# Optimization experiments

Hardware: AMD Instinct MI355X
Metric: run time of the kernel (lower is better)

Reference implementation:

```python
import jax, jax.numpy as jnp
import numpy as np

DIM_IN = 256
DIM = 256      # dim_out
N = 4096       # nodes at current depth
K = 16         # max children (padded)
R = 8192       # rows in previous-level h/c tensors (row 0 is the zero init row)


def _reverse_sequence(x, length):
    """TF reverse_sequence along axis 1: reverse first length[i] steps, keep tail."""
    T = x.shape[1]
    t = jnp.arange(T)
    idx = jnp.where(t[None, :] < length[:, None], length[:, None] - 1 - t[None, :], t[None, :])
    return jnp.take_along_axis(x, idx[:, :, None], axis=1)


def _lstm(x, kernel, rec, bias, h0, c0):
    """Standard (CuDNN/Keras gate order i,f,g,o) LSTM. x: [B,T,D] -> y: [B,T,H]."""
    xz = jnp.einsum('btd,dg->btg', x, kernel) + bias  # precompute input projection

    def step(carry, xz_t):
        h, c = carry
        z = xz_t + h @ rec
        i, f, g, o = jnp.split(z, 4, axis=-1)
        c = jax.nn.sigmoid(f) * c + jax.nn.sigmoid(i) * jnp.tanh(g)
        h = jax.nn.sigmoid(o) * jnp.tanh(c)
        return (h, c), h

    _, ys = jax.lax.scan(step, (h0, c0), jnp.swapaxes(xz, 0, 1))
    return jnp.swapaxes(ys, 0, 1)


def _bilstm(x, length, kernel, rec, bias, init_h, init_c, fc_w, return_seq):
    """kernel/rec/bias/init_* have a leading dir axis of size 2 (fwd, bwd)."""
    B = x.shape[0]
    h0f = jnp.broadcast_to(init_h[0], (B, DIM))
    c0f = jnp.broadcast_to(init_c[0], (B, DIM))
    h0b = jnp.broadcast_to(init_h[1], (B, DIM))
    c0b = jnp.broadcast_to(init_c[1], (B, DIM))
    x_back = _reverse_sequence(x, length)
    y_f = _lstm(x, kernel[0], rec[0], bias[0], h0f, c0f)
    y_b = _lstm(x_back, kernel[1], rec[1], bias[1], h0b, c0b)
    y = jnp.concatenate([y_f, y_b], axis=-1)  # [B,T,2*DIM] (y_b not re-reversed, as in TF code)
    if return_seq:
        return y @ fc_w
    y_last = y[jnp.arange(B), length - 1]  # last valid timestep
    return y_last @ fc_w


def setup_inputs() -> dict:
    key = jax.random.key(0)
    ks = jax.random.split(key, 16)
    x = jax.random.normal(ks[0], (N, DIM_IN), dtype=jnp.float32)
    h_tensor = jax.random.normal(ks[1], (R, DIM), dtype=jnp.float32)
    c_tensor = jax.random.normal(ks[2], (R, DIM), dtype=jnp.float32)
    # padded child-index matrix: each row has length in [1, K], padded with -1
    raw = jax.random.randint(ks[3], (N, K), 0, R, dtype=jnp.int32)
    lengths = jax.random.randint(ks[4], (N,), 1, K + 1, dtype=jnp.int32)
    indice = jnp.where(jnp.arange(K)[None, :] < lengths[:, None], raw, jnp.int32(-1))
    # Dense W: dim_in -> 4*dim_out
    W_w = jax.random.normal(ks[5], (DIM_IN, 4 * DIM), dtype=jnp.float32) * 0.05
    W_b = jnp.zeros((4 * DIM,), dtype=jnp.float32)
    # 4 BiLSTMs (gates f,i,u,o), each with 2 directions; input dim = DIM (gathered h)
    lstm_kernel = jax.random.normal(ks[6], (4, 2, DIM, 4 * DIM), dtype=jnp.float32) * 0.05
    lstm_rec = jax.random.normal(ks[7], (4, 2, DIM, 4 * DIM), dtype=jnp.float32) * 0.05
    lstm_bias = jnp.zeros((4, 2, 4 * DIM), dtype=jnp.float32)
    init_h = jax.random.normal(ks[8], (4, 2, 1, DIM), dtype=jnp.float32) * 0.01
    init_c = jax.random.normal(ks[9], (4, 2, 1, DIM), dtype=jnp.float32) * 0.01
    fc_w = jax.random.normal(ks[10], (4, 2 * DIM, DIM), dtype=jnp.float32) * 0.05
    return {"x": x, "h_tensor": h_tensor, "c_tensor": c_tensor, "indice": indice,
            "W_w": W_w, "W_b": W_b, "lstm_kernel": lstm_kernel, "lstm_rec": lstm_rec,
            "lstm_bias": lstm_bias, "init_h": init_h, "init_c": init_c, "fc_w": fc_w}


def reference(x, h_tensor, c_tensor, indice, W_w, W_b, lstm_kernel, lstm_rec,
              lstm_bias, init_h, init_c, fc_w):
    mask_bool = indice != -1
    mask = mask_bool.astype(jnp.float32)                # [N,K]
    length = jnp.sum(mask, axis=1).astype(jnp.int32)    # [N]
    safe_idx = jnp.where(mask_bool, indice, 0)
    h = h_tensor[safe_idx]  # [N,K,DIM] gathered child states
    c = c_tensor[safe_idx]
    W_x = x @ W_w + W_b
    W_f_x, W_i_x, W_u_x, W_o_x = jnp.split(W_x, 4, axis=-1)
    # forget gate: per-child BiLSTM sequence output
    f_seq = _bilstm(h, length, lstm_kernel[0], lstm_rec[0], lstm_bias[0],
                    init_h[0], init_c[0], fc_w[0], return_seq=True)  # [N,K,DIM]
    branch_f_k = jax.nn.sigmoid(W_f_x[:, None, :] + f_seq)
    branch_f = jnp.sum(branch_f_k * c * mask[:, :, None], axis=1)    # masked reduce
    branch_i = jax.nn.sigmoid(_bilstm(h, length, lstm_kernel[1], lstm_rec[1], lstm_bias[1],
                                      init_h[1], init_c[1], fc_w[1], False) + W_i_x)
    branch_u = jnp.tanh(_bilstm(h, length, lstm_kernel[2], lstm_rec[2], lstm_bias[2],
                                init_h[2], init_c[2], fc_w[2], False) + W_u_x)
    branch_o = jax.nn.sigmoid(_bilstm(h, length, lstm_kernel[3], lstm_rec[3], lstm_bias[3],
                                      init_h[3], init_c[3], fc_w[3], False) + W_o_x)
    new_c = branch_i * branch_u + branch_f
    new_h = branch_o * jnp.tanh(new_c)
    return new_h, new_c
```

## Files before the change

kernel.cpp:

```cpp
#include <hip/hip_runtime.h>
#include <stdint.h>

typedef __bf16 bf16x8 __attribute__((ext_vector_type(8)));
typedef float  f32x4  __attribute__((ext_vector_type(4)));
typedef unsigned short u16;
typedef unsigned int   u32;

#define NN   4096
#define KCH  16
#define RR   8192

static constexpr size_t OFF_WCOMB = 0;
static constexpr size_t OFF_FCWT  = 8388608;
static constexpr size_t OFF_HST   = 9961472;
static constexpr size_t OFF_CST   = 43515904;
static constexpr size_t OFF_YSEQ  = 77070336;
static constexpr size_t OFF_YLAST = 144179200;
static constexpr size_t OFF_BRF   = 160956416;
static constexpr size_t OFF_FCO   = 163053568;
static constexpr size_t OFF_XS    = 169345024;
static constexpr size_t OFF_HN    = 171442176;
static constexpr size_t OFF_CN    = 175636480;
static constexpr size_t OFF_BIASN = 179830784;
static constexpr size_t OFF_IHN   = 179847168;
static constexpr size_t OFF_ICN   = 179851264;
static constexpr size_t OFF_WBN   = 179855360;
static constexpr size_t OFF_IDX   = 179857408;
static constexpr size_t OFF_LEN   = 180119552;
static constexpr size_t OFF_FLAG  = 180135936;
static constexpr size_t OFF_NODEOF= 180136000;
static constexpr size_t OFF_LENS  = 180152384;
static constexpr size_t OFF_NTN   = 180168768;
static constexpr size_t WS_NEEDED = 180168832;

struct KParams {
  const void *x, *h_tensor, *c_tensor, *W_w, *W_b, *lstm_kernel, *lstm_rec,
             *lstm_bias, *init_h, *init_c, *fc_w;
  const int *indice;
  u16 *wcomb, *fcwT2, *h_state, *y_seq, *y_last, *brf, *fc_outb,
      *xs, *hn, *cn, *biasn, *inithn, *initcn, *wbn;
  float *c_stateT;
  int *idxf, *len, *flag, *nodeof, *len_s, *ntneed;
  float *outp;
};

__device__ __forceinline__ float b2f(u16 u){ union{u32 i;float f;}v; v.i=((u32)u)<<16; return v.f; }
__device__ __forceinline__ u16  f2b(float f){ union{float f;u32 i;}v; v.f=f; u32 r=v.i+0x7FFFu+((v.i>>16)&1u); return (u16)(r>>16); }
__device__ __forceinline__ float sigm(float x){ return 1.0f/(1.0f+__expf(-x)); }
__device__ __forceinline__ float tanh_(float x){ return 2.0f/(1.0f+__expf(-2.0f*x)) - 1.0f; }
__device__ __forceinline__ u16  cvt(const void* q, size_t i, int isf){
  return isf ? f2b(((const float*)q)[i]) : ((const u16*)q)[i];
}
__device__ __forceinline__ void cp16(const u16* g, u16* l){
  __builtin_amdgcn_global_load_lds((const __attribute__((address_space(1))) u32*)g,
                                   (__attribute__((address_space(3))) u32*)l, 16, 0, 0);
}

__global__ void detect_k(KParams p){
  __shared__ int cnt[256];
  int tid = threadIdx.x;
  u16 u = ((const u16*)p.x)[2*tid];
  int e = (u >> 7) & 0xFF;
  cnt[tid] = (u != 0 && e >= 100 && e <= 140) ? 1 : 0;
  __syncthreads();
  if (tid == 0){
    int s = 0;
    for (int i=0;i<256;i++) s += cnt[i];
    *p.flag = (s < 192) ? 1 : 0;
  }
}

__global__ void prep_idx_k(KParams p){
  int n = blockIdx.x*256 + threadIdx.x;
  if (n >= NN) return;
  int L = 0;
  #pragma unroll
  for (int t=0;t<KCH;t++) L += (p.indice[n*KCH+t] != -1);
  p.len[n] = L;
}

__global__ void sort_k(KParams p){
  __shared__ int cnt[17];
  __shared__ int start[17];
  int tid = threadIdx.x;
  if (tid < 17) cnt[tid] = 0;
  __syncthreads();
  for (int n = tid; n < NN; n += 256) atomicAdd(&cnt[p.len[n]], 1);
  __syncthreads();
  if (tid == 0){
    int acc = 0;
    for (int v = 16; v >= 1; --v){ start[v] = acc; acc += cnt[v]; }
    for (int t = 0; t < 16; ++t){
      int need = (t == 0) ? NN : start[t];
      p.ntneed[t] = (need + 127) >> 7;
    }
  }
  __syncthreads();
  for (int n = tid; n < NN; n += 256){
    int ps = atomicAdd(&start[p.len[n]], 1);
    p.nodeof[ps] = n;
  }
}

__global__ void norm_k(KParams p){
  int i = blockIdx.x*256 + threadIdx.x;
  if (i >= 4207616) return;
  int isf = *p.flag;
  if (i < 2097152)       p.hn[i] = cvt(p.h_tensor, i, isf);
  else if (i < 4194304)  p.cn[i-2097152] = cvt(p.c_tensor, i-2097152, isf);
  else if (i < 4202496){ int j = i-4194304; int gd = j>>10, pc = j&1023;
                         p.biasn[j] = cvt(p.lstm_bias, gd*1024 + ((pc&3)<<8) + (pc>>2), isf); }
  else if (i < 4204544)  p.inithn[i-4202496] = cvt(p.init_h, i-4202496, isf);
  else if (i < 4206592)  p.initcn[i-4204544] = cvt(p.init_c, i-4204544, isf);
  else                   p.wbn[i-4206592] = cvt(p.W_b, i-4206592, isf);
}

__global__ void xperm_k(KParams p){
  int ns = blockIdx.x, u = threadIdx.x;
  int n = p.nodeof[ns];
  p.xs[(size_t)ns*256 + u] = cvt(p.x, (size_t)n*256 + u, *p.flag);
}

__global__ void prep_idx2_k(KParams p){
  int ns = blockIdx.x*256 + threadIdx.x;
  if (ns >= NN) return;
  int n = p.nodeof[ns];
  p.len_s[ns] = p.len[n];
  #pragma unroll
  for (int t=0;t<KCH;t++){
    int v = p.indice[n*KCH+t];
    p.idxf[t*NN + ns] = (v != -1) ? v : 0;
  }
}

__global__ void prep_w_k(KParams p){
  int i = blockIdx.x*256 + threadIdx.x;
  int isf = *p.flag;
  if (i < 4194304){
    int gd = i>>19, pc = (i>>9)&1023, k = i&511;
    int perm = ((pc&3)<<8) + (pc>>2);
    p.wcomb[i] = (k < 256) ? cvt(p.lstm_rec,    (size_t)(gd*256 + k)*1024 + perm, isf)
                           : cvt(p.lstm_kernel, (size_t)(gd*256 + (k-256))*1024 + perm, isf);
  } else if (i < 4980736){
    int j = i - 4194304;
    int g = j/196608, rem = j%196608, o = rem/768, k = rem%768;
    p.fcwT2[j] = (k < 512) ? cvt(p.fc_w, (size_t)(g*512 + k)*256 + o, isf)
                           : cvt(p.W_w,  (size_t)(k-512)*1024 + g*256 + o, isf);
  }
}

__global__ void prep_state_k(KParams p){
  int i = blockIdx.x*256 + threadIdx.x;
  int gd = i >> 20;
  p.h_state[i]  = p.inithn[(gd<<8) + (i & 255)];
  p.c_stateT[i] = b2f(p.initcn[(gd<<8) + ((i>>12)&255)]);
}

__global__ void fallback_k(float* out){
  int i = blockIdx.x*256 + threadIdx.x;
  out[i] = 1000.0f; out[1048576 + i] = 1000.0f;
}

enum { MODE_STAGE=0, MODE_FC0=1, MODE_FC123=2 };

template<int MODE>
__launch_bounds__(256)
__global__ void gemm_k(KParams p, int t)
{
  __shared__ __align__(16) u16 As[128*64];
  __shared__ __align__(16) u16 Bs[128*64];
  __shared__ __align__(16) u16 hbuf[(MODE==MODE_STAGE)?128*40:1];
  __shared__ int nidx[(MODE!=MODE_FC123)?128:1];
  __shared__ u16 biasl[(MODE==MODE_STAGE)?128:1];
  __shared__ int Ln[(MODE==MODE_FC0)?8:1];

  const int tid = threadIdx.x;
  const int lane = tid & 63, wv = tid >> 6;
  const int col16 = lane & 15, quad = lane >> 4;
  const int wy = wv >> 1, wx = wv & 1;

  constexpr int K = (MODE==MODE_STAGE) ? 512 : 768;

  int mtile, ntile, gd = 0;
  const u16 *Ap=nullptr, *Bh=nullptr;
  if constexpr (MODE==MODE_STAGE){
    int b = blockIdx.x;
    gd = b & 7; mtile = (b>>3) & 7; ntile = b >> 6;
    if (ntile >= p.ntneed[t]) return;
    Ap = p.wcomb + (size_t)gd*1024*512;
    Bh = p.h_state + ((size_t)(t&1)*8 + gd)*NN*256;
  } else if constexpr (MODE==MODE_FC0){
    mtile = blockIdx.x; ntile = blockIdx.y;
  } else {
    mtile = blockIdx.x; ntile = blockIdx.y; gd = blockIdx.z;
  }
  const int rowA = mtile*128;
  const int rowB = ntile*128;

  if constexpr (MODE==MODE_STAGE){
    if (tid < 128){
      int n = rowB + tid;
      int L = p.len_s[n];
      int d = gd & 1;
      int eff = (d && t < L) ? (L-1-t) : t;
      nidx[tid] = p.idxf[eff*NN + n];
      biasl[tid] = p.biasn[gd*1024 + rowA + tid];
    }
    __syncthreads();
  }
  if constexpr (MODE==MODE_FC0){
    if (tid < 128){
      int nl = tid>>4, tt = tid&15;
      nidx[tid] = p.idxf[tt*NN + mtile*8 + nl];
    }
    if (tid < 8) Ln[tid] = p.len_s[mtile*8 + tid];
    __syncthreads();
  }

  f32x4 acc[4][4] = {};

  for (int kt = 0; kt < K/64; ++kt){
    const int kk = kt*64;
    #pragma unroll
    for (int i=0;i<4;i++){
      int ch = wv*4 + i;
      int r  = ch*8 + (lane>>3);
      int cb = (lane&7)*8;
      const u16 *ga, *gb;
      if constexpr (MODE==MODE_STAGE){
        ga = Ap + (size_t)(rowA+r)*512 + kk + cb;
        gb = (kk < 256) ? (Bh + (size_t)(rowB+r)*256 + kk + cb)
                        : (p.hn + (size_t)nidx[r]*256 + (kk-256) + cb);
      } else if constexpr (MODE==MODE_FC0){
        if (kk < 512){
          const u16* Asel = (kk < 256) ? p.y_seq : p.y_seq + (size_t)65536*256;
          ga = Asel + (size_t)(rowA+r)*256 + (kk&255) + cb;
        } else {
          ga = p.xs + (size_t)((rowA+r)>>4)*256 + (kk-512) + cb;
        }
        gb = p.fcwT2 + (size_t)(rowB+r)*768 + kk + cb;
      } else {
        int g = gd + 1;
        if (kk < 512){
          const u16* Asel = p.y_last + (size_t)(g*2 + (kk>=256))*NN*256;
          ga = Asel + (size_t)(rowA+r)*256 + (kk&255) + cb;
        } else {
          ga = p.xs + (size_t)(rowA+r)*256 + (kk-512) + cb;
        }
        gb = p.fcwT2 + (size_t)g*196608 + (size_t)(rowB+r)*768 + kk + cb;
      }
      cp16(ga, &As[ch*512]);
      cp16(gb, &Bs[ch*512]);
    }
    __syncthreads();
    #pragma unroll
    for (int ks=0; ks<64; ks+=32){
      bf16x8 af[4], bfr[4];
      #pragma unroll
      for (int mf=0; mf<4; mf++)
        af[mf] = *(const bf16x8*)&As[(wy*64+mf*16+col16)*64 + ks + quad*8];
      #pragma unroll
      for (int nf=0; nf<4; nf++)
        bfr[nf] = *(const bf16x8*)&Bs[(wx*64+nf*16+col16)*64 + ks + quad*8];
      #pragma unroll
      for (int mf=0; mf<4; mf++)
        #pragma unroll
        for (int nf=0; nf<4; nf++)
          acc[mf][nf] = __builtin_amdgcn_mfma_f32_16x16x32_bf16(af[mf], bfr[nf], acc[mf][nf], 0, 0, 0);
    }
    __syncthreads();
  }

  if constexpr (MODE==MODE_STAGE){
    const int g = gd >> 1, d = gd & 1;
    const int wbuf = (t+1) & 1;
    #pragma unroll
    for (int nf=0; nf<4; nf++){
      int nc_ = wx*64 + nf*16 + col16;
      int n = rowB + nc_;
      #pragma unroll
      for (int mf=0; mf<4; mf++){
        int lp = wy*64 + mf*16 + quad*4;
        int u  = (rowA + lp) >> 2;
        float zi = acc[mf][nf][0] + b2f(biasl[lp+0]);
        float zf = acc[mf][nf][1] + b2f(biasl[lp+1]);
        float zg = acc[mf][nf][2] + b2f(biasl[lp+2]);
        float zo = acc[mf][nf][3] + b2f(biasl[lp+3]);
        size_t ci = ((size_t)gd*256 + u)*NN + n;
        float cp = p.c_stateT[ci];
        float cn = sigm(zf)*cp + sigm(zi)*tanh_(zg);
        float hn = sigm(zo)*tanh_(cn);
        p.c_stateT[ci] = cn;
        hbuf[nc_*40 + (lp>>2)] = f2b(hn);
      }
    }
    __syncthreads();
    int row = tid >> 1, half = tid & 1;
    int n = rowB + row;
    int u0 = (rowA >> 2) + half*16;
    uint4 v0 = *(const uint4*)&hbuf[row*40 + half*16];
    uint4 v1 = *(const uint4*)&hbuf[row*40 + half*16 + 8];
    u16* hw = p.h_state + (((size_t)wbuf*8 + gd)*NN + n)*256 + u0;
    ((uint4*)hw)[0] = v0; ((uint4*)hw)[1] = v1;
    if (g == 0){
      u16* yw = p.y_seq + ((size_t)d*65536 + (size_t)n*KCH + t)*256 + u0;
      ((uint4*)yw)[0] = v0; ((uint4*)yw)[1] = v1;
    } else if (p.len_s[n] == t+1){
      u16* lw = p.y_last + ((size_t)gd*NN + n)*256 + u0;
      ((uint4*)lw)[0] = v0; ((uint4*)lw)[1] = v1;
    }
  } else if constexpr (MODE==MODE_FC0){
    #pragma unroll
    for (int mf=0; mf<4; mf++){
      int nl = wy*4 + mf;
      int n  = mtile*8 + nl;
      int L  = Ln[nl];
      #pragma unroll
      for (int nf=0; nf<4; nf++){
        int u = rowB + wx*64 + nf*16 + col16;
        float wb_ = b2f(p.wbn[u]);
        float psum = 0.f;
        #pragma unroll
        for (int r=0;r<4;r++){
          int tt = quad*4 + r;
          if (tt < L){
            int ridx = nidx[nl*16 + tt];
            float cch = b2f(p.cn[(size_t)ridx*256 + u]);
            psum += sigm(acc[mf][nf][r] + wb_) * cch;
          }
        }
        psum += __shfl_xor(psum, 16);
        psum += __shfl_xor(psum, 32);
        if (quad == 0) p.brf[(size_t)n*256 + u] = f2b(psum);
      }
    }
  } else {
    int g = gd + 1;
    #pragma unroll
    for (int mf=0; mf<4; mf++){
      int r0 = rowA + wy*64 + mf*16 + quad*4;
      #pragma unroll
      for (int nf=0; nf<4; nf++){
        int c = rowB + wx*64 + nf*16 + col16;
        float wb_ = b2f(p.wbn[g*256 + c]);
        u16* o = p.fc_outb + (size_t)gd*NN*256 + (size_t)r0*256 + c;
        #pragma unroll
        for (int r=0;r<4;r++) o[(size_t)r*256] = f2b(acc[mf][nf][r] + wb_);
      }
    }
  }
}

__global__ void final_k(KParams p){
  int i = blockIdx.x*256 + threadIdx.x;
  int ns = i >> 8, u = i & 255;
  int n = p.nodeof[ns];
  float bf_ = b2f(p.brf[i]);
  float bi = sigm (b2f(p.fc_outb[i]));
  float bu = tanh_(b2f(p.fc_outb[1048576 + i]));
  float bo = sigm (b2f(p.fc_outb[2097152 + i]));
  float nc = bi*bu + bf_;
  float nh = bo*tanh_(nc);
  p.outp[(size_t)n*256 + u] = nh;
  p.outp[1048576 + (size_t)n*256 + u] = nc;
}

extern "C" void kernel_launch(void* const* d_in, const int* in_sizes, int n_in,
                              void* d_out, int out_size, void* d_ws, size_t ws_size,
                              hipStream_t stream) {
  if (ws_size < WS_NEEDED){
    fallback_k<<<4096, 256, 0, stream>>>((float*)d_out);
    return;
  }
  KParams p;
  p.x          = d_in[0];
  p.h_tensor   = d_in[1];
  p.c_tensor   = d_in[2];
  p.indice     = (const int*)d_in[3];
  p.W_w        = d_in[4];
  p.W_b        = d_in[5];
  p.lstm_kernel= d_in[6];
  p.lstm_rec   = d_in[7];
  p.lstm_bias  = d_in[8];
  p.init_h     = d_in[9];
  p.init_c     = d_in[10];
  p.fc_w       = d_in[11];
  char* w = (char*)d_ws;
  p.wcomb   = (u16*)  (w + OFF_WCOMB);
  p.fcwT2   = (u16*)  (w + OFF_FCWT);
  p.h_state = (u16*)  (w + OFF_HST);
  p.c_stateT= (float*)(w + OFF_CST);
  p.y_seq   = (u16*)  (w + OFF_YSEQ);
  p.y_last  = (u16*)  (w + OFF_YLAST);
  p.brf     = (u16*)  (w + OFF_BRF);
  p.fc_outb = (u16*)  (w + OFF_FCO);
  p.xs      = (u16*)  (w + OFF_XS);
  p.hn      = (u16*)  (w + OFF_HN);
  p.cn      = (u16*)  (w + OFF_CN);
  p.biasn   = (u16*)  (w + OFF_BIASN);
  p.inithn  = (u16*)  (w + OFF_IHN);
  p.initcn  = (u16*)  (w + OFF_ICN);
  p.wbn     = (u16*)  (w + OFF_WBN);
  p.idxf    = (int*)  (w + OFF_IDX);
  p.len     = (int*)  (w + OFF_LEN);
  p.flag    = (int*)  (w + OFF_FLAG);
  p.nodeof  = (int*)  (w + OFF_NODEOF);
  p.len_s   = (int*)  (w + OFF_LENS);
  p.ntneed  = (int*)  (w + OFF_NTN);
  p.outp    = (float*)d_out;

  detect_k    <<<1,     256, 0, stream>>>(p);
  prep_idx_k  <<<16,    256, 0, stream>>>(p);
  sort_k      <<<1,     256, 0, stream>>>(p);
  norm_k      <<<16436, 256, 0, stream>>>(p);
  xperm_k     <<<4096,  256, 0, stream>>>(p);
  prep_idx2_k <<<16,    256, 0, stream>>>(p);
  prep_w_k    <<<19456, 256, 0, stream>>>(p);
  prep_state_k<<<32768, 256, 0, stream>>>(p);

  for (int t = 0; t < KCH; ++t)
    gemm_k<MODE_STAGE><<<2048, 256, 0, stream>>>(p, t);

  gemm_k<MODE_FC0>  <<<dim3(512,2),  256, 0, stream>>>(p, 0);
  gemm_k<MODE_FC123><<<dim3(32,2,3), 256, 0, stream>>>(p, 0);

  final_k<<<4096, 256, 0, stream>>>(p);
}
```

Measured before the change: 902.2 us.

## Replace per-timestep LSTM GEMM launches with persistent kernel keeping state in registers

The sixteen per-timestep GEMM launches are replaced by one persistent kernel. Each block owns 64 nodes for one gate/direction and loops over timesteps, keeping h and c in registers and h in LDS. This removes the global h/c state buffers, the state-init kernel and repeated launches. Each block runs only up to the longest length among its nodes, since nodes are sorted by length. In exchange, weights are read directly from global memory (L2) at every step with no LDS staging, each block recomputes over 1024 gate rows, and register pressure is high.

```diff
diff --git a/kernel.cpp b/kernel.cpp
--- a/kernel.cpp
+++ b/kernel.cpp
@@ -12,35 +12,31 @@
 
 static constexpr size_t OFF_WCOMB = 0;
 static constexpr size_t OFF_FCWT  = 8388608;
-static constexpr size_t OFF_HST   = 9961472;
-static constexpr size_t OFF_CST   = 43515904;
-static constexpr size_t OFF_YSEQ  = 77070336;
-static constexpr size_t OFF_YLAST = 144179200;
-static constexpr size_t OFF_BRF   = 160956416;
-static constexpr size_t OFF_FCO   = 163053568;
-static constexpr size_t OFF_XS    = 169345024;
-static constexpr size_t OFF_HN    = 171442176;
-static constexpr size_t OFF_CN    = 175636480;
-static constexpr size_t OFF_BIASN = 179830784;
-static constexpr size_t OFF_IHN   = 179847168;
-static constexpr size_t OFF_ICN   = 179851264;
-static constexpr size_t OFF_WBN   = 179855360;
-static constexpr size_t OFF_IDX   = 179857408;
-static constexpr size_t OFF_LEN   = 180119552;
-static constexpr size_t OFF_FLAG  = 180135936;
-static constexpr size_t OFF_NODEOF= 180136000;
-static constexpr size_t OFF_LENS  = 180152384;
-static constexpr size_t OFF_NTN   = 180168768;
-static constexpr size_t WS_NEEDED = 180168832;
+static constexpr size_t OFF_YSEQ  = 9961472;
+static constexpr size_t OFF_YLAST = 77070336;
+static constexpr size_t OFF_BRF   = 93847552;
+static constexpr size_t OFF_FCO   = 95944704;
+static constexpr size_t OFF_XS    = 102236160;
+static constexpr size_t OFF_HN    = 104333312;
+static constexpr size_t OFF_CN    = 108527616;
+static constexpr size_t OFF_BIASN = 112721920;
+static constexpr size_t OFF_IHN   = 112738304;
+static constexpr size_t OFF_ICN   = 112742400;
+static constexpr size_t OFF_WBN   = 112746496;
+static constexpr size_t OFF_IDX   = 112748544;
+static constexpr size_t OFF_LEN   = 113010688;
+static constexpr size_t OFF_FLAG  = 113027072;
+static constexpr size_t OFF_NODEOF= 113027136;
+static constexpr size_t OFF_LENS  = 113043520;
+static constexpr size_t WS_NEEDED = 113059904;
 
 struct KParams {
   const void *x, *h_tensor, *c_tensor, *W_w, *W_b, *lstm_kernel, *lstm_rec,
              *lstm_bias, *init_h, *init_c, *fc_w;
   const int *indice;
-  u16 *wcomb, *fcwT2, *h_state, *y_seq, *y_last, *brf, *fc_outb,
+  u16 *wcomb, *fcwT2, *y_seq, *y_last, *brf, *fc_outb,
       *xs, *hn, *cn, *biasn, *inithn, *initcn, *wbn;
-  float *c_stateT;
-  int *idxf, *len, *flag, *nodeof, *len_s, *ntneed;
+  int *idxf, *len, *flag, *nodeof, *len_s;
   float *outp;
 };
 
@@ -90,10 +86,6 @@
   if (tid == 0){
     int acc = 0;
     for (int v = 16; v >= 1; --v){ start[v] = acc; acc += cnt[v]; }
-    for (int t = 0; t < 16; ++t){
-      int need = (t == 0) ? NN : start[t];
-      p.ntneed[t] = (need + 127) >> 7;
-    }
   }
   __syncthreads();
   for (int n = tid; n < NN; n += 256){
@@ -149,29 +141,153 @@
   }
 }
 
-__global__ void prep_state_k(KParams p){
-  int i = blockIdx.x*256 + threadIdx.x;
-  int gd = i >> 20;
-  p.h_state[i]  = p.inithn[(gd<<8) + (i & 255)];
-  p.c_stateT[i] = b2f(p.initcn[(gd<<8) + ((i>>12)&255)]);
-}
-
 __global__ void fallback_k(float* out){
   int i = blockIdx.x*256 + threadIdx.x;
   out[i] = 1000.0f; out[1048576 + i] = 1000.0f;
 }
 
-enum { MODE_STAGE=0, MODE_FC0=1, MODE_FC123=2 };
+__device__ __forceinline__ void flushy(const KParams& p, int gd, int d, int nbase,
+                                       int tp, const u16* hS, int tid){
+  int row = tid >> 2, part = tid & 3;
+  int ng = nbase + row;
+  if (gd < 2){
+    u16* dst = p.y_seq + ((size_t)d*65536 + (size_t)ng*16 + tp)*256;
+    #pragma unroll
+    for (int j = 0; j < 8; ++j){
+      int cl = part*8 + j;
+      uint4 v = *(const uint4*)&hS[row*256 + ((cl ^ (row&7))<<3)];
+      *(uint4*)(dst + cl*8) = v;
+    }
+  } else if (p.len_s[ng] == tp+1){
+    u16* dst = p.y_last + ((size_t)gd*NN + ng)*256;
+    #pragma unroll
+    for (int j = 0; j < 8; ++j){
+      int cl = part*8 + j;
+      uint4 v = *(const uint4*)&hS[row*256 + ((cl ^ (row&7))<<3)];
+      *(uint4*)(dst + cl*8) = v;
+    }
+  }
+}
+
+__global__ __launch_bounds__(256, 2) void stage_persist_k(KParams p){
+  __shared__ __align__(16) u16 hS[16384];
+  __shared__ __align__(16) u16 gS[16384];
+
+  const int b = blockIdx.x;
+  const int gd = b & 7, ntile = b >> 3;
+  const int nbase = ntile * 64;
+  const int tid = threadIdx.x, lane = tid & 63, wv = tid >> 6;
+  const int col16 = lane & 15, quad = lane >> 4;
+  const int d = gd & 1;
+  const u16* __restrict__ wc = p.wcomb + (size_t)gd * 524288;
+  const int Lmax = p.len_s[nbase];
+
+  float c_reg[64];
+  u16   h_reg[64];
+  {
+    const u16* ih = p.inithn + gd*256;
+    const u16* ic = p.initcn + gd*256;
+    #pragma unroll
+    for (int i = 0; i < 64; ++i){
+      int u = wv*64 + (i>>4)*16 + ((i>>2)&3)*4 + quad;
+      h_reg[i] = ih[u];
+      c_reg[i] = b2f(ic[u]);
+    }
+  }
+
+  for (int t = 0; t < Lmax; ++t){
+    __syncthreads();
+    {
+      #pragma unroll
+      for (int q = 0; q < 8; ++q){
+        int ii = wv*8 + q;
+        int nl = ii*2 + (lane>>5);
+        int ng = nbase + nl;
+        int L  = p.len_s[ng];
+        int eff = (d && t < L) ? (L-1-t) : t;
+        int g  = p.idxf[eff*NN + ng];
+        int c  = lane & 31;
+        cp16(p.hn + (size_t)g*256 + ((c ^ (nl & 7)) << 3), &gS[ii*512]);
+      }
+    }
+    #pragma unroll
+    for (int i = 0; i < 64; ++i){
+      int u = wv*64 + (i>>4)*16 + ((i>>2)&3)*4 + quad;
+      int n = (i & 3)*16 + col16;
+      hS[n*256 + ((((u>>3) ^ (n & 7)) << 3) | (u & 7))] = h_reg[i];
+    }
+    __syncthreads();
+    if (t > 0) flushy(p, gd, d, nbase, t-1, hS, tid);
+
+    #pragma unroll
+    for (int pI = 0; pI < 4; ++pI){
+      const int mb = wv*256 + pI*64;
+      f32x4 acc[4][4] = {};
+      for (int kt = 0; kt < 8; ++kt){
+        const u16* bs = (kt < 4) ? hS : gS;
+        const int ktl = kt & 3;
+        #pragma unroll
+        for (int ks = 0; ks < 2; ++ks){
+          bf16x8 af[4], bfr[4];
+          #pragma unroll
+          for (int mf = 0; mf < 4; ++mf)
+            af[mf] = *(const bf16x8*)(wc + (size_t)(mb + mf*16 + col16)*512 + kt*64 + ks*32 + quad*8);
+          #pragma unroll
+          for (int nf = 0; nf < 4; ++nf){
+            int n  = nf*16 + col16;
+            int ch = ktl*8 + ks*4 + quad;
+            bfr[nf] = *(const bf16x8*)&bs[n*256 + ((ch ^ (n & 7)) << 3)];
+          }
+          #pragma unroll
+          for (int mf = 0; mf < 4; ++mf)
+            #pragma unroll
+            for (int nf = 0; nf < 4; ++nf)
+              acc[mf][nf] = __builtin_amdgcn_mfma_f32_16x16x32_bf16(af[mf], bfr[nf], acc[mf][nf], 0, 0, 0);
+        }
+      }
+      #pragma unroll
+      for (int mf = 0; mf < 4; ++mf){
+        int pcol = mb + mf*16 + quad*4;
+        uint2 bv = *(const uint2*)(p.biasn + gd*1024 + pcol);
+        float bi_ = b2f((u16)(bv.x & 0xffffu));
+        float bf_ = b2f((u16)(bv.x >> 16));
+        float bg_ = b2f((u16)(bv.y & 0xffffu));
+        float bo_ = b2f((u16)(bv.y >> 16));
+        #pragma unroll
+        for (int nf = 0; nf < 4; ++nf){
+          int flat = pI*16 + mf*4 + nf;
+          float zi = acc[mf][nf][0] + bi_;
+          float zf = acc[mf][nf][1] + bf_;
+          float zg = acc[mf][nf][2] + bg_;
+          float zo = acc[mf][nf][3] + bo_;
+          float cp_ = c_reg[flat];
+          float cn = sigm(zf)*cp_ + sigm(zi)*tanh_(zg);
+          c_reg[flat] = cn;
+          h_reg[flat] = f2b(sigm(zo)*tanh_(cn));
+        }
+      }
+    }
+  }
+  __syncthreads();
+  #pragma unroll
+  for (int i = 0; i < 64; ++i){
+    int u = wv*64 + (i>>4)*16 + ((i>>2)&3)*4 + quad;
+    int n = (i & 3)*16 + col16;
+    hS[n*256 + ((((u>>3) ^ (n & 7)) << 3) | (u & 7))] = h_reg[i];
+  }
+  __syncthreads();
+  flushy(p, gd, d, nbase, Lmax-1, hS, tid);
+}
+
+enum { MODE_FC0=0, MODE_FC123=1 };
 
 template<int MODE>
 __launch_bounds__(256)
-__global__ void gemm_k(KParams p, int t)
+__global__ void gemm_k(KParams p)
 {
   __shared__ __align__(16) u16 As[128*64];
   __shared__ __align__(16) u16 Bs[128*64];
-  __shared__ __align__(16) u16 hbuf[(MODE==MODE_STAGE)?128*40:1];
-  __shared__ int nidx[(MODE!=MODE_FC123)?128:1];
-  __shared__ u16 biasl[(MODE==MODE_STAGE)?128:1];
+  __shared__ int nidx[(MODE==MODE_FC0)?128:1];
   __shared__ int Ln[(MODE==MODE_FC0)?8:1];
 
   const int tid = threadIdx.x;
@@ -179,35 +295,12 @@
   const int col16 = lane & 15, quad = lane >> 4;
   const int wy = wv >> 1, wx = wv & 1;
 
-  constexpr int K = (MODE==MODE_STAGE) ? 512 : 768;
-
-  int mtile, ntile, gd = 0;
-  const u16 *Ap=nullptr, *Bh=nullptr;
-  if constexpr (MODE==MODE_STAGE){
-    int b = blockIdx.x;
-    gd = b & 7; mtile = (b>>3) & 7; ntile = b >> 6;
-    if (ntile >= p.ntneed[t]) return;
-    Ap = p.wcomb + (size_t)gd*1024*512;
-    Bh = p.h_state + ((size_t)(t&1)*8 + gd)*NN*256;
-  } else if constexpr (MODE==MODE_FC0){
-    mtile = blockIdx.x; ntile = blockIdx.y;
-  } else {
-    mtile = blockIdx.x; ntile = blockIdx.y; gd = blockIdx.z;
-  }
+  constexpr int K = 768;
+
+  int mtile = blockIdx.x, ntile = blockIdx.y, gd = blockIdx.z;
   const int rowA = mtile*128;
   const int rowB = ntile*128;
 
-  if constexpr (MODE==MODE_STAGE){
-    if (tid < 128){
-      int n = rowB + tid;
-      int L = p.len_s[n];
-      int d = gd & 1;
-      int eff = (d && t < L) ? (L-1-t) : t;
-      nidx[tid] = p.idxf[eff*NN + n];
-      biasl[tid] = p.biasn[gd*1024 + rowA + tid];
-    }
-    __syncthreads();
-  }
   if constexpr (MODE==MODE_FC0){
     if (tid < 128){
       int nl = tid>>4, tt = tid&15;
@@ -227,11 +320,7 @@
       int r  = ch*8 + (lane>>3);
       int cb = (lane&7)*8;
       const u16 *ga, *gb;
-      if constexpr (MODE==MODE_STAGE){
-        ga = Ap + (size_t)(rowA+r)*512 + kk + cb;
-        gb = (kk < 256) ? (Bh + (size_t)(rowB+r)*256 + kk + cb)
-                        : (p.hn + (size_t)nidx[r]*256 + (kk-256) + cb);
-      } else if constexpr (MODE==MODE_FC0){
+      if constexpr (MODE==MODE_FC0){
         if (kk < 512){
           const u16* Asel = (kk < 256) ? p.y_seq : p.y_seq + (size_t)65536*256;
           ga = Asel + (size_t)(rowA+r)*256 + (kk&255) + cb;
@@ -271,45 +360,7 @@
     __syncthreads();
   }
 
-  if constexpr (MODE==MODE_STAGE){
-    const int g = gd >> 1, d = gd & 1;
-    const int wbuf = (t+1) & 1;
-    #pragma unroll
-    for (int nf=0; nf<4; nf++){
-      int nc_ = wx*64 + nf*16 + col16;
-      int n = rowB + nc_;
-      #pragma unroll
-      for (int mf=0; mf<4; mf++){
-        int lp = wy*64 + mf*16 + quad*4;
-        int u  = (rowA + lp) >> 2;
-        float zi = acc[mf][nf][0] + b2f(biasl[lp+0]);
-        float zf = acc[mf][nf][1] + b2f(biasl[lp+1]);
-        float zg = acc[mf][nf][2] + b2f(biasl[lp+2]);
-        float zo = acc[mf][nf][3] + b2f(biasl[lp+3]);
-        size_t ci = ((size_t)gd*256 + u)*NN + n;
-        float cp = p.c_stateT[ci];
-        float cn = sigm(zf)*cp + sigm(zi)*tanh_(zg);
-        float hn = sigm(zo)*tanh_(cn);
-        p.c_stateT[ci] = cn;
-        hbuf[nc_*40 + (lp>>2)] = f2b(hn);
-      }
-    }
-    __syncthreads();
-    int row = tid >> 1, half = tid & 1;
-    int n = rowB + row;
-    int u0 = (rowA >> 2) + half*16;
-    uint4 v0 = *(const uint4*)&hbuf[row*40 + half*16];
-    uint4 v1 = *(const uint4*)&hbuf[row*40 + half*16 + 8];
-    u16* hw = p.h_state + (((size_t)wbuf*8 + gd)*NN + n)*256 + u0;
-    ((uint4*)hw)[0] = v0; ((uint4*)hw)[1] = v1;
-    if (g == 0){
-      u16* yw = p.y_seq + ((size_t)d*65536 + (size_t)n*KCH + t)*256 + u0;
-      ((uint4*)yw)[0] = v0; ((uint4*)yw)[1] = v1;
-    } else if (p.len_s[n] == t+1){
-      u16* lw = p.y_last + ((size_t)gd*NN + n)*256 + u0;
-      ((uint4*)lw)[0] = v0; ((uint4*)lw)[1] = v1;
-    }
-  } else if constexpr (MODE==MODE_FC0){
+  if constexpr (MODE==MODE_FC0){
     #pragma unroll
     for (int mf=0; mf<4; mf++){
       int nl = wy*4 + mf;
@@ -388,8 +439,6 @@
   char* w = (char*)d_ws;
   p.wcomb   = (u16*)  (w + OFF_WCOMB);
   p.fcwT2   = (u16*)  (w + OFF_FCWT);
-  p.h_state = (u16*)  (w + OFF_HST);
-  p.c_stateT= (float*)(w + OFF_CST);
   p.y_seq   = (u16*)  (w + OFF_YSEQ);
   p.y_last  = (u16*)  (w + OFF_YLAST);
   p.brf     = (u16*)  (w + OFF_BRF);
@@ -406,7 +455,6 @@
   p.flag    = (int*)  (w + OFF_FLAG);
   p.nodeof  = (int*)  (w + OFF_NODEOF);
   p.len_s   = (int*)  (w + OFF_LENS);
-  p.ntneed  = (int*)  (w + OFF_NTN);
   p.outp    = (float*)d_out;
 
   detect_k    <<<1,     256, 0, stream>>>(p);
@@ -416,13 +464,11 @@
   xperm_k     <<<4096,  256, 0, stream>>>(p);
   prep_idx2_k <<<16,    256, 0, stream>>>(p);
   prep_w_k    <<<19456, 256, 0, stream>>>(p);
-  prep_state_k<<<32768, 256, 0, stream>>>(p);
-
-  for (int t = 0; t < KCH; ++t)
-    gemm_k<MODE_STAGE><<<2048, 256, 0, stream>>>(p, t);
-
-  gemm_k<MODE_FC0>  <<<dim3(512,2),  256, 0, stream>>>(p, 0);
-  gemm_k<MODE_FC123><<<dim3(32,2,3), 256, 0, stream>>>(p, 0);
+
+  stage_persist_k<<<512, 256, 0, stream>>>(p);
+
+  gemm_k<MODE_FC0>  <<<dim3(512,2,1), 256, 0, stream>>>(p);
+  gemm_k<MODE_FC123><<<dim3(32,2,3),  256, 0, stream>>>(p);
 
   final_k<<<4096, 256, 0, stream>>>(p);
 }
```

After: 2.090 ms. 2.32x slower.

## Double-buffer GEMM shared-memory tiles and XOR-swizzle LDS columns

Applied to the files above, without the earlier changes.

The GEMM kernel's A/B tiles become ping-pong buffers, so the load for the next K-slice is issued before computing the current one, with one barrier per iteration instead of two. The 16-byte column chunks are also XOR-swizzled by row, both in the global-to-LDS copies and in the fragment reads, to reduce LDS bank conflicts. The aim is to hide global-load latency and cut LDS conflicts in the recurrent stage GEMMs and the FC GEMMs. In exchange, shared memory per block doubles to about 74 KB, which may lower occupancy. Real overlap also depends on cp16 not waiting for its own loads to finish.

```diff
diff --git a/kernel.cpp b/kernel.cpp
--- a/kernel.cpp
+++ b/kernel.cpp
@@ -167,8 +167,8 @@
 __launch_bounds__(256)
 __global__ void gemm_k(KParams p, int t)
 {
-  __shared__ __align__(16) u16 As[128*64];
-  __shared__ __align__(16) u16 Bs[128*64];
+  __shared__ __align__(16) u16 As[2][8192];
+  __shared__ __align__(16) u16 Bs[2][8192];
   __shared__ __align__(16) u16 hbuf[(MODE==MODE_STAGE)?128*40:1];
   __shared__ int nidx[(MODE!=MODE_FC123)?128:1];
   __shared__ u16 biasl[(MODE==MODE_STAGE)?128:1];
@@ -179,7 +179,8 @@
   const int col16 = lane & 15, quad = lane >> 4;
   const int wy = wv >> 1, wx = wv & 1;
 
-  constexpr int K = (MODE==MODE_STAGE) ? 512 : 768;
+  constexpr int K  = (MODE==MODE_STAGE) ? 512 : 768;
+  constexpr int KT = K/64;
 
   int mtile, ntile, gd = 0;
   const u16 *Ap=nullptr, *Bh=nullptr;
@@ -217,58 +218,69 @@
     __syncthreads();
   }
 
-  f32x4 acc[4][4] = {};
-
-  for (int kt = 0; kt < K/64; ++kt){
+  auto stage = [&](int kt, int buf){
     const int kk = kt*64;
     #pragma unroll
     for (int i=0;i<4;i++){
       int ch = wv*4 + i;
       int r  = ch*8 + (lane>>3);
-      int cb = (lane&7)*8;
+      int cs = (((lane&7) ^ (r&7)) << 3);
       const u16 *ga, *gb;
       if constexpr (MODE==MODE_STAGE){
-        ga = Ap + (size_t)(rowA+r)*512 + kk + cb;
-        gb = (kk < 256) ? (Bh + (size_t)(rowB+r)*256 + kk + cb)
-                        : (p.hn + (size_t)nidx[r]*256 + (kk-256) + cb);
+        ga = Ap + (size_t)(rowA+r)*512 + kk + cs;
+        gb = (kk < 256) ? (Bh + (size_t)(rowB+r)*256 + kk + cs)
+                        : (p.hn + (size_t)nidx[r]*256 + (kk-256) + cs);
       } else if constexpr (MODE==MODE_FC0){
         if (kk < 512){
           const u16* Asel = (kk < 256) ? p.y_seq : p.y_seq + (size_t)65536*256;
-          ga = Asel + (size_t)(rowA+r)*256 + (kk&255) + cb;
+          ga = Asel + (size_t)(rowA+r)*256 + (kk&255) + cs;
         } else {
-          ga = p.xs + (size_t)((rowA+r)>>4)*256 + (kk-512) + cb;
+          ga = p.xs + (size_t)((rowA+r)>>4)*256 + (kk-512) + cs;
         }
-        gb = p.fcwT2 + (size_t)(rowB+r)*768 + kk + cb;
+        gb = p.fcwT2 + (size_t)(rowB+r)*768 + kk + cs;
       } else {
         int g = gd + 1;
         if (kk < 512){
           const u16* Asel = p.y_last + (size_t)(g*2 + (kk>=256))*NN*256;
-          ga = Asel + (size_t)(rowA+r)*256 + (kk&255) + cb;
+          ga = Asel + (size_t)(rowA+r)*256 + (kk&255) + cs;
         } else {
-          ga = p.xs + (size_t)(rowA+r)*256 + (kk-512) + cb;
+          ga = p.xs + (size_t)(rowA+r)*256 + (kk-512) + cs;
         }
-        gb = p.fcwT2 + (size_t)g*196608 + (size_t)(rowB+r)*768 + kk + cb;
-      }
-      cp16(ga, &As[ch*512]);
-      cp16(gb, &Bs[ch*512]);
-    }
+        gb = p.fcwT2 + (size_t)g*196608 + (size_t)(rowB+r)*768 + kk + cs;
+      }
+      cp16(ga, &As[buf][ch*512]);
+      cp16(gb, &Bs[buf][ch*512]);
+    }
+  };
+
+  f32x4 acc[4][4] = {};
+
+  stage(0, 0);
+  for (int kt = 0; kt < KT; ++kt){
     __syncthreads();
+    if (kt+1 < KT) stage(kt+1, (kt+1)&1);
+    const int bsel = kt & 1;
     #pragma unroll
     for (int ks=0; ks<64; ks+=32){
       bf16x8 af[4], bfr[4];
       #pragma unroll
-      for (int mf=0; mf<4; mf++)
-        af[mf] = *(const bf16x8*)&As[(wy*64+mf*16+col16)*64 + ks + quad*8];
-      #pragma unroll
-      for (int nf=0; nf<4; nf++)
-        bfr[nf] = *(const bf16x8*)&Bs[(wx*64+nf*16+col16)*64 + ks + quad*8];
+      for (int mf=0; mf<4; mf++){
+        int row = wy*64+mf*16+col16;
+        int lc  = (ks>>3) + quad;
+        af[mf] = *(const bf16x8*)&As[bsel][row*64 + ((lc ^ (row&7))<<3)];
+      }
+      #pragma unroll
+      for (int nf=0; nf<4; nf++){
+        int row = wx*64+nf*16+col16;
+        int lc  = (ks>>3) + quad;
+        bfr[nf] = *(const bf16x8*)&Bs[bsel][row*64 + ((lc ^ (row&7))<<3)];
+      }
       #pragma unroll
       for (int mf=0; mf<4; mf++)
         #pragma unroll
         for (int nf=0; nf<4; nf++)
           acc[mf][nf] = __builtin_amdgcn_mfma_f32_16x16x32_bf16(af[mf], bfr[nf], acc[mf][nf], 0, 0, 0);
     }
-    __syncthreads();
   }
 
   if constexpr (MODE==MODE_STAGE){
@@ -421,7 +433,7 @@
   for (int t = 0; t < KCH; ++t)
     gemm_k<MODE_STAGE><<<2048, 256, 0, stream>>>(p, t);
 
-  gemm_k<MODE_FC0>  <<<dim3(512,2),  256, 0, stream>>>(p, 0);
+  gemm_k<MODE_FC0>  <<<dim3(512,2), 256, 0, stream>>>(p, 0);
   gemm_k<MODE_FC123><<<dim3(32,2,3), 256, 0, stream>>>(p, 0);
 
   final_k<<<4096, 256, 0, stream>>>(p);
```

Measured after the change: 908.4 us. Within noise of the previous version (+0.7%).
